# Performance work log

Measured on AMD Instinct MI355X. Metric: run time of the kernel, lower is better.

## Reference

```python
import jax, jax.numpy as jnp
import numpy as np
from jax import lax

EPS = 1e-5

def _dsconv(x, dw, pw, g, b, m, v, relu):
    # x: [B,C,H,W]; dw: [C,1,3,3] depthwise; pw: [C,C,1,1] pointwise; eval-mode BN
    C = x.shape[1]
    y = lax.conv_general_dilated(x, dw, (1, 1), 'SAME', feature_group_count=C)
    y = lax.conv_general_dilated(y, pw, (1, 1), 'SAME')
    scale = (g * lax.rsqrt(v + EPS))[None, :, None, None]
    y = y * scale + (b - m * g * lax.rsqrt(v + EPS))[None, :, None, None]
    return jnp.maximum(y, 0.0) if relu else y

def _attention(x, wq, bq, wk, bk, wv, bv, gamma):
    b, c, h, w = x.shape
    n = h * w
    xf = x.reshape(b, c, n)                      # [B,C,N]
    q = jnp.einsum('oc,bcn->bon', wq, xf) + bq[None, :, None]   # [B,C/8,N]
    k = jnp.einsum('oc,bcn->bon', wk, xf) + bk[None, :, None]   # [B,C/8,N]
    v = jnp.einsum('oc,bcn->bon', wv, xf) + bv[None, :, None]   # [B,C,N]
    logits = jnp.einsum('bdm,bdn->bmn', q, k)    # q^T k, [B,N,N]
    attn = jax.nn.softmax(logits, axis=2)
    out = jnp.einsum('bcn,bmn->bcm', v, attn).reshape(b, c, h, w)
    return gamma[0] * out + x

def setup_inputs() -> dict:
    key = jax.random.key(0)
    ks = jax.random.split(key, 20)
    B, C, H, W = 64, 256, 32, 32
    C8 = C // 8
    rn = lambda k, s, sc: (jax.random.normal(k, s, dtype=jnp.float32) * sc)
    return {
        'x': rn(ks[0], (B, C, H, W), 1.0),
        'dw1': rn(ks[1], (C, 1, 3, 3), 0.2),
        'pw1': rn(ks[2], (C, C, 1, 1), 0.06),
        'bn1_g': jax.random.uniform(ks[3], (C,), jnp.float32, 0.5, 1.5),
        'bn1_b': rn(ks[4], (C,), 0.1),
        'bn1_m': rn(ks[5], (C,), 0.1),
        'bn1_v': jax.random.uniform(ks[6], (C,), jnp.float32, 0.5, 1.5),
        'dw2': rn(ks[7], (C, 1, 3, 3), 0.2),
        'pw2': rn(ks[8], (C, C, 1, 1), 0.06),
        'bn2_g': jax.random.uniform(ks[9], (C,), jnp.float32, 0.5, 1.5),
        'bn2_b': rn(ks[10], (C,), 0.1),
        'bn2_m': rn(ks[11], (C,), 0.1),
        'bn2_v': jax.random.uniform(ks[12], (C,), jnp.float32, 0.5, 1.5),
        'wq': rn(ks[13], (C8, C), 0.06),
        'bq': rn(ks[14], (C8,), 0.02),
        'wk': rn(ks[15], (C8, C), 0.06),
        'bk': rn(ks[16], (C8,), 0.02),
        'wv': rn(ks[17], (C, C), 0.06),
        'bv': rn(ks[18], (C,), 0.02),
        'gamma': rn(ks[19], (1,), 0.5),
    }

def reference(x, dw1, pw1, bn1_g, bn1_b, bn1_m, bn1_v,
              dw2, pw2, bn2_g, bn2_b, bn2_m, bn2_v,
              wq, bq, wk, bk, wv, bv, gamma):
    out = _dsconv(x, dw1, pw1, bn1_g, bn1_b, bn1_m, bn1_v, relu=True)
    out = _dsconv(out, dw2, pw2, bn2_g, bn2_b, bn2_m, bn2_v, relu=False)
    out = _attention(out + x, wq, bq, wk, bk, wv, bv, gamma)
    return jnp.maximum(out, 0.0)
```

## Files before the change

### kernel.cpp

```cpp
#include <hip/hip_runtime.h>
#include <cstdint>
#include <cstddef>

#define B_ 64
#define C_ 256
#define N_ 1024
#define LOG2E 1.4426950408889634f

typedef short v8s __attribute__((ext_vector_type(8)));
typedef float v4f __attribute__((ext_vector_type(4)));
typedef unsigned int u32;
typedef unsigned short u16;

#define VMCNT(N) asm volatile("s_waitcnt vmcnt(" #N ")" ::: "memory")
#define LGKM0 asm volatile("s_waitcnt lgkmcnt(0)" ::: "memory")
#define SBAR __builtin_amdgcn_s_barrier()
#define SCHEDB __builtin_amdgcn_sched_barrier(0)

__device__ __forceinline__ float bf2f(u16 u) {
  return __uint_as_float(((u32)u) << 16);
}
__device__ __forceinline__ u16 f2bf(float f) {
  u32 x = __float_as_uint(f);
  x += 0x7fffu + ((x >> 16) & 1u);
  return (u16)(x >> 16);
}
__device__ __forceinline__ u32 pack2(float a, float b) {
  return (u32)f2bf(a) | ((u32)f2bf(b) << 16);
}
__device__ __forceinline__ u32 cvtpk(float lo, float hi) {
  u32 r;
  asm("v_cvt_pk_bf16_f32 %0, %1, %2" : "=v"(r) : "v"(lo), "v"(hi));
  return r;
}

typedef __attribute__((address_space(3))) unsigned int lds_as_t;
typedef __attribute__((address_space(1))) const unsigned int glb_as_t;
__device__ __forceinline__ void ld_lds16(const u16* g, u16* l) {
  __builtin_amdgcn_global_load_lds((glb_as_t*)g, (lds_as_t*)l, 16, 0, 0);
}

__global__ __launch_bounds__(256) void prep(
    const float* __restrict__ g1, const float* __restrict__ b1,
    const float* __restrict__ m1, const float* __restrict__ v1,
    const float* __restrict__ g2, const float* __restrict__ b2,
    const float* __restrict__ m2, const float* __restrict__ v2,
    const float* __restrict__ wq, const float* __restrict__ bq,
    const float* __restrict__ wk, const float* __restrict__ bk,
    const float* __restrict__ wv, const float* __restrict__ bv,
    const float* __restrict__ pw1, const float* __restrict__ pw2,
    const float* __restrict__ dw1, const float* __restrict__ dw2,
    float* __restrict__ scale1, float* __restrict__ shift1,
    float* __restrict__ scale2, float* __restrict__ shift2,
    float* __restrict__ dwT1, float* __restrict__ dwT2,
    u16* __restrict__ pw1b, u16* __restrict__ pw2b, u16* __restrict__ wcatb,
    float* __restrict__ bcat) {
  const int gt = blockIdx.x * 256 + threadIdx.x;
  if (gt < 256) {
    float s1 = g1[gt] * rsqrtf(v1[gt] + 1e-5f);
    scale1[gt] = s1;
    shift1[gt] = b1[gt] - m1[gt] * s1;
    float s2 = g2[gt] * rsqrtf(v2[gt] + 1e-5f);
    scale2[gt] = s2;
    shift2[gt] = b2[gt] - m2[gt] * s2;
  }
  if (gt < 320)
    bcat[gt] = (gt < 32) ? bq[gt] * LOG2E
                         : (gt < 64) ? bk[gt - 32] : bv[gt - 64];
  if (gt < 2304) {
    dwT1[(gt % 9) * 256 + gt / 9] = dw1[gt];
    dwT2[(gt % 9) * 256 + gt / 9] = dw2[gt];
  }
  for (int e = gt; e < 65536; e += 16384) {
    pw1b[e] = f2bf(pw1[e]);
    pw2b[e] = f2bf(pw2[e]);
  }
  for (int e = gt; e < 81920; e += 16384) {
    const int o = e >> 8;
    float w = (o < 32) ? wq[e] * LOG2E
                       : (o < 64) ? wk[e - 8192] : wv[e - 16384];
    wcatb[e] = f2bf(w);
  }
}

__global__ __launch_bounds__(256) void transpose_x(const float* __restrict__ x,
                                                   u16* __restrict__ xt) {
  __shared__ float t[64][65];
  const int b = blockIdx.z, c0 = blockIdx.y * 64, n0 = blockIdx.x * 64;
  const float* xp = x + ((size_t)b * C_ + c0) * N_ + n0;
  const int tn = threadIdx.x & 63, tc = threadIdx.x >> 6;
#pragma unroll
  for (int i = 0; i < 16; ++i)
    t[tc + 4 * i][tn] = xp[(size_t)(tc + 4 * i) * N_ + tn];
  __syncthreads();
  u16* op = xt + ((size_t)b * N_ + n0) * C_ + c0;
  const int oc = threadIdx.x & 63, on = threadIdx.x >> 6;
#pragma unroll
  for (int i = 0; i < 16; ++i)
    op[(size_t)(on + 4 * i) * C_ + oc] = f2bf(t[oc][on + 4 * i]);
}

__global__ __launch_bounds__(256) void dw_nhwc(const u16* __restrict__ src,
                                               const float* __restrict__ wT,
                                               u16* __restrict__ dst) {
  __shared__ float wl[9][256];
  const int b = blockIdx.y;
  for (int e = threadIdx.x; e < 2304; e += 256) wl[e >> 8][e & 255] = wT[e];
  __syncthreads();
  const int pl = threadIdx.x >> 5, c0 = (threadIdx.x & 31) * 8;
  const int p = blockIdx.x * 8 + pl;
  const int h = p >> 5, wx = p & 31;
  const u16* sp = src + (size_t)b * N_ * C_;
  float acc[8] = {0.f, 0.f, 0.f, 0.f, 0.f, 0.f, 0.f, 0.f};
#pragma unroll
  for (int dh = -1; dh <= 1; ++dh) {
    const int hh = h + dh;
    if (hh < 0 || hh > 31) continue;
#pragma unroll
    for (int dx = -1; dx <= 1; ++dx) {
      const int ww = wx + dx;
      if (ww < 0 || ww > 31) continue;
      const int k = (dh + 1) * 3 + (dx + 1);
      const uint4 v = *(const uint4*)(sp + (size_t)(hh * 32 + ww) * C_ + c0);
      const u32 vv[4] = {v.x, v.y, v.z, v.w};
#pragma unroll
      for (int j = 0; j < 4; ++j) {
        acc[2 * j] += bf2f((u16)(vv[j] & 0xffffu)) * wl[k][c0 + 2 * j];
        acc[2 * j + 1] += bf2f((u16)(vv[j] >> 16)) * wl[k][c0 + 2 * j + 1];
      }
    }
  }
  uint4 o4;
  o4.x = pack2(acc[0], acc[1]);
  o4.y = pack2(acc[2], acc[3]);
  o4.z = pack2(acc[4], acc[5]);
  o4.w = pack2(acc[6], acc[7]);
  *(uint4*)(dst + ((size_t)b * N_ + p) * C_ + c0) = o4;
}

template <int EPI>
__global__ __launch_bounds__(256, 4) void gemm(
    const u16* __restrict__ X, const u16* __restrict__ W,
    const float* __restrict__ scale, const float* __restrict__ shift,
    const u16* __restrict__ resid, u16* __restrict__ Y, u16* __restrict__ Y2) {
  __shared__ u16 smem[17408];
  u16(*Ys)[136] = (u16(*)[136])smem;
  u16(*YsQ)[68] = (u16(*)[68])smem;

  const int tid = threadIdx.x;
  const int b = blockIdx.z;
  const int n0 = blockIdx.x * 128, o0 = blockIdx.y * 128;
  const int wid = tid >> 6, lane = tid & 63;
  const int wn = wid & 1, wo = wid >> 1;
  const int l15 = lane & 15, l4 = lane >> 4;
  const int r16 = lane >> 2, c16 = (lane & 3) * 8;

  v4f acc[4][4];
#pragma unroll
  for (int i = 0; i < 4; ++i)
#pragma unroll
    for (int j = 0; j < 4; ++j) acc[i][j] = v4f{0.f, 0.f, 0.f, 0.f};

  auto stage = [&](int kidx, int bufsel) {
    const int k0 = (kidx & 7) * 32;
    u16* Xd = smem + bufsel * 8192;
    u16* Wd = Xd + 4096;
#pragma unroll
    for (int g = 0; g < 2; ++g) {
      const int base = wid * 32 + g * 16;
      ld_lds16(X + ((size_t)b * N_ + n0 + base + r16) * C_ + k0 + c16,
               Xd + base * 32);
      int wr = o0 + base + r16;
      if (EPI == 2 && wr > 319) wr = 319;
      ld_lds16(W + (size_t)wr * C_ + k0 + c16, Wd + base * 32);
    }
  };

  stage(0, 0);
  stage(1, 1);

#pragma unroll
  for (int k = 0; k < 8; ++k) {
    const int cur = k & 1;
    if (k < 7) {
      VMCNT(4);
    } else {
      VMCNT(0);
    }
    SCHEDB;
    SBAR;
    const u16(*Xs)[32] = (const u16(*)[32])(smem + cur * 8192);
    const u16(*Ws)[32] = (const u16(*)[32])(smem + cur * 8192 + 4096);
    v8s af[4], bf4[4];
#pragma unroll
    for (int f = 0; f < 4; ++f) {
      if constexpr (EPI != 2) {
        af[f] = *(const v8s*)&Ws[wo * 64 + f * 16 + l15][l4 * 8];
        bf4[f] = *(const v8s*)&Xs[wn * 64 + f * 16 + l15][l4 * 8];
      } else {
        af[f] = *(const v8s*)&Xs[wn * 64 + f * 16 + l15][l4 * 8];
        bf4[f] = *(const v8s*)&Ws[wo * 64 + f * 16 + l15][l4 * 8];
      }
    }
#pragma unroll
    for (int i = 0; i < 4; ++i)
#pragma unroll
      for (int j = 0; j < 4; ++j)
        acc[i][j] = __builtin_amdgcn_mfma_f32_16x16x32_bf16(af[i], bf4[j],
                                                            acc[i][j], 0, 0, 0);
    LGKM0;
    SBAR;
    SCHEDB;
    if (k < 6) stage(k + 2, cur);
  }

  if constexpr (EPI != 2) {
#pragma unroll
    for (int i = 0; i < 4; ++i) {
      const int oL = wo * 64 + i * 16 + l4 * 4;
      const int o = o0 + oL;
      const float4 sc = *(const float4*)&scale[o];
      const float4 sh = *(const float4*)&shift[o];
#pragma unroll
      for (int j = 0; j < 4; ++j) {
        const int nL = wn * 64 + j * 16 + l15;
        float y0 = acc[i][j][0] * sc.x + sh.x;
        float y1 = acc[i][j][1] * sc.y + sh.y;
        float y2 = acc[i][j][2] * sc.z + sh.z;
        float y3 = acc[i][j][3] * sc.w + sh.w;
        if constexpr (EPI == 0) {
          y0 = fmaxf(y0, 0.f);
          y1 = fmaxf(y1, 0.f);
          y2 = fmaxf(y2, 0.f);
          y3 = fmaxf(y3, 0.f);
        } else {
          const uint2 rb =
              *(const uint2*)(resid + ((size_t)b * N_ + n0 + nL) * C_ + o);
          y0 += bf2f((u16)(rb.x & 0xffffu));
          y1 += bf2f((u16)(rb.x >> 16));
          y2 += bf2f((u16)(rb.y & 0xffffu));
          y3 += bf2f((u16)(rb.y >> 16));
        }
        uint2 st;
        st.x = pack2(y0, y1);
        st.y = pack2(y2, y3);
        *(uint2*)&Ys[nL][oL] = st;
      }
    }
    __syncthreads();
#pragma unroll
    for (int s = 0; s < 8; ++s) {
      const int nL = s * 16 + (tid >> 4);
      const int slot = tid & 15;
      const uint4 v = *(const uint4*)&Ys[nL][slot * 8];
      *(uint4*)&Y[((size_t)b * N_ + n0 + nL) * C_ + o0 + slot * 8] = v;
    }
  } else {
    float bj[4];
#pragma unroll
    for (int j = 0; j < 4; ++j) {
      int o = o0 + wo * 64 + j * 16 + l15;
      bj[j] = shift[o > 319 ? 319 : o];
    }
    if (o0 == 0 && wo == 0) {
#pragma unroll
      for (int i = 0; i < 4; ++i) {
        const int nL = wn * 64 + i * 16 + l4 * 4;
#pragma unroll
        for (int j = 0; j < 4; ++j) {
          const int oL = j * 16 + l15;
#pragma unroll
          for (int r = 0; r < 4; ++r)
            YsQ[nL + r][oL] = f2bf(acc[i][j][r] + bj[j]);
        }
      }
    } else {
#pragma unroll
      for (int i = 0; i < 4; ++i) {
        const int nL = wn * 64 + i * 16 + l4 * 4;
#pragma unroll
        for (int j = 0; j < 4; ++j) {
          const int oL = wo * 64 + j * 16 + l15;
          uint2 st;
          st.x = pack2(acc[i][j][0] + bj[j], acc[i][j][1] + bj[j]);
          st.y = pack2(acc[i][j][2] + bj[j], acc[i][j][3] + bj[j]);
          *(uint2*)&Ys[oL][nL] = st;
        }
      }
    }
    __syncthreads();
    if (o0 == 0) {
#pragma unroll
      for (int s = 0; s < 4; ++s) {
        const int e = s * 256 + tid;
        const int row = e >> 3, seg = e & 7;
        const uint4 v = *(const uint4*)&YsQ[row][seg * 8];
        *(uint4*)&Y[((size_t)b * N_ + n0 + row) * 64 + seg * 8] = v;
      }
#pragma unroll
      for (int s = 0; s < 4; ++s) {
        const int e = s * 256 + tid;
        const int oL = 64 + (e >> 4), slot = e & 15;
        const uint4 v = *(const uint4*)&Ys[oL][slot * 8];
        *(uint4*)&Y2[((size_t)b * C_ + oL - 64) * N_ + n0 + slot * 8] = v;
      }
    } else {
#pragma unroll
      for (int s = 0; s < 8; ++s) {
        const int oL = s * 16 + (tid >> 4);
        const int c = o0 + oL - 64;
        if (c < 256) {
          const int slot = tid & 15;
          const uint4 v = *(const uint4*)&Ys[oL][slot * 8];
          *(uint4*)&Y2[((size_t)b * C_ + c) * N_ + n0 + slot * 8] = v;
        }
      }
    }
  }
}

__global__ __launch_bounds__(256, 3) void flash(
    const u16* __restrict__ qk, const u16* __restrict__ vchw,
    const u16* __restrict__ abf, const float* __restrict__ gamma_p,
    float* __restrict__ out) {
  const int b = blockIdx.x;
  const int m0 = blockIdx.y * 64;
  const int tid = threadIdx.x, wid = tid >> 6, lane = tid & 63;
  const int l15 = lane & 15, l4 = lane >> 4;
  const int mw = m0 + wid * 16;
  const int cq = wid * 64;

  __shared__ u16 Vs[256][64];
  __shared__ u16 Pl[2][64][72];
  __shared__ float Sl[64];

  const u16* qkb = qk + (size_t)b * N_ * 64;
  const u16* vb = vchw + (size_t)b * C_ * N_;
  const v8s qf = *(const v8s*)&qkb[(size_t)(mw + l15) * 64 + l4 * 8];

  const int s_row = lane >> 3;
  const int s_j = (lane & 7) ^ (s_row & 7);

#pragma unroll
  for (int g = 0; g < 8; ++g) {
    const int base = cq + g * 8;
    ld_lds16(vb + (size_t)(base + s_row) * N_ + s_j * 8, &Vs[base][0]);
  }

  float Mloc = -3e38f;
  {
    v8s kf[4];
#pragma unroll
    for (int f = 0; f < 4; ++f)
      kf[f] = *(const v8s*)&qkb[(size_t)(f * 16 + l15) * 64 + 32 + l4 * 8];
    for (int t = 0; t < 16; ++t) {
      v8s kn[4];
      if (t < 15) {
        const int n1 = (t + 1) * 64;
#pragma unroll
        for (int f = 0; f < 4; ++f)
          kn[f] =
              *(const v8s*)&qkb[(size_t)(n1 + f * 16 + l15) * 64 + 32 + l4 * 8];
      }
#pragma unroll
      for (int f = 0; f < 4; ++f) {
        const v4f lt = __builtin_amdgcn_mfma_f32_16x16x32_bf16(
            kf[f], qf, v4f{0.f, 0.f, 0.f, 0.f}, 0, 0, 0);
        Mloc = fmaxf(Mloc, fmaxf(fmaxf(lt[0], lt[1]), fmaxf(lt[2], lt[3])));
      }
      if (t < 15) {
#pragma unroll
        for (int f = 0; f < 4; ++f) kf[f] = kn[f];
      }
    }
  }
  Mloc = fmaxf(Mloc, __shfl_xor(Mloc, 16));
  Mloc = fmaxf(Mloc, __shfl_xor(Mloc, 32));
  const float M = Mloc;

  v4f acc[4][4];
#pragma unroll
  for (int mf = 0; mf < 4; ++mf)
#pragma unroll
    for (int j = 0; j < 4; ++j) acc[mf][j] = v4f{0.f, 0.f, 0.f, 0.f};
  float S0 = 0.f, S1 = 0.f, S2 = 0.f, S3 = 0.f;
  v8s kf[4];
#pragma unroll
  for (int f = 0; f < 4; ++f)
    kf[f] = *(const v8s*)&qkb[(size_t)(f * 16 + l15) * 64 + 32 + l4 * 8];
  VMCNT(0);

  for (int t = 0; t < 16; ++t) {
    const int tb = t & 1;
    v4f lt[4];
#pragma unroll
    for (int f = 0; f < 4; ++f)
      lt[f] = __builtin_amdgcn_mfma_f32_16x16x32_bf16(
          kf[f], qf, v4f{0.f, 0.f, 0.f, 0.f}, 0, 0, 0);
#pragma unroll
    for (int f = 0; f < 4; ++f) {
      const float p0 = exp2f(lt[f][0] - M);
      const float p1 = exp2f(lt[f][1] - M);
      const float p2 = exp2f(lt[f][2] - M);
      const float p3 = exp2f(lt[f][3] - M);
      S0 += p0;
      S1 += p1;
      S2 += p2;
      S3 += p3;
      uint2 pw;
      pw.x = cvtpk(p0, p1);
      pw.y = cvtpk(p2, p3);
      *(uint2*)&Pl[tb][wid * 16 + l15][f * 16 + l4 * 4] = pw;
    }
    SCHEDB;
    {
      const int n1 = ((t + 1) & 15) * 64;
#pragma unroll
      for (int f = 0; f < 4; ++f)
        kf[f] =
            *(const v8s*)&qkb[(size_t)(n1 + f * 16 + l15) * 64 + 32 + l4 * 8];
    }
    SCHEDB;
    LGKM0;
    SBAR;
    VMCNT(4);
    SCHEDB;
    __builtin_amdgcn_s_setprio(1);
#pragma unroll
    for (int ks = 0; ks < 2; ++ks) {
      v8s pa[4];
#pragma unroll
      for (int mf = 0; mf < 4; ++mf)
        pa[mf] = *(const v8s*)&Pl[tb][mf * 16 + l15][ks * 32 + l4 * 8];
#pragma unroll
      for (int j = 0; j < 4; ++j) {
        const int col = 8 * (((ks * 4) + l4) ^ (l15 & 7));
        const v8s vf = *(const v8s*)&Vs[cq + j * 16 + l15][col];
#pragma unroll
        for (int mf = 0; mf < 4; ++mf)
          acc[mf][j] = __builtin_amdgcn_mfma_f32_16x16x32_bf16(
              pa[mf], vf, acc[mf][j], 0, 0, 0);
      }
    }
    __builtin_amdgcn_s_setprio(0);
    SCHEDB;
    {
      const int n1 = ((t + 1) & 15) * 64;
#pragma unroll
      for (int g = 0; g < 8; ++g) {
        const int base = cq + g * 8;
        ld_lds16(vb + (size_t)(base + s_row) * N_ + n1 + s_j * 8, &Vs[base][0]);
      }
    }
    SCHEDB;
  }

  float S = (S0 + S1) + (S2 + S3);
  S += __shfl_xor(S, 16);
  S += __shfl_xor(S, 32);
  if (lane < 16) Sl[wid * 16 + lane] = 1.f / S;
  __syncthreads();

  const float gma = gamma_p[0];
  float invv[4][4];
#pragma unroll
  for (int mf = 0; mf < 4; ++mf)
#pragma unroll
    for (int r = 0; r < 4; ++r) invv[mf][r] = Sl[mf * 16 + l4 * 4 + r];

#pragma unroll
  for (int mf = 0; mf < 4; ++mf) {
    const int mb = m0 + mf * 16 + l4 * 4;
#pragma unroll
    for (int j = 0; j < 4; ++j) {
      const int c = cq + j * 16 + l15;
      float4 y;
      float* yp = (float*)&y;
#pragma unroll
      for (int r = 0; r < 4; ++r) {
        const float av = bf2f(abf[((size_t)b * N_ + mb + r) * C_ + c]);
        yp[r] = fmaxf(gma * acc[mf][j][r] * invv[mf][r] + av, 0.f);
      }
      *(float4*)&out[((size_t)b * C_ + c) * N_ + mb] = y;
    }
  }
}

extern "C" void kernel_launch(void* const* d_in, const int* in_sizes, int n_in,
                              void* d_out, int out_size, void* d_ws,
                              size_t ws_size, hipStream_t stream) {
  const float* x = (const float*)d_in[0];
  const float* dw1 = (const float*)d_in[1];
  const float* pw1 = (const float*)d_in[2];
  const float* bn1g = (const float*)d_in[3];
  const float* bn1b = (const float*)d_in[4];
  const float* bn1m = (const float*)d_in[5];
  const float* bn1v = (const float*)d_in[6];
  const float* dw2 = (const float*)d_in[7];
  const float* pw2 = (const float*)d_in[8];
  const float* bn2g = (const float*)d_in[9];
  const float* bn2b = (const float*)d_in[10];
  const float* bn2m = (const float*)d_in[11];
  const float* bn2v = (const float*)d_in[12];
  const float* wq = (const float*)d_in[13];
  const float* bq = (const float*)d_in[14];
  const float* wk = (const float*)d_in[15];
  const float* bk = (const float*)d_in[16];
  const float* wv = (const float*)d_in[17];
  const float* bv = (const float*)d_in[18];
  const float* gamma = (const float*)d_in[19];
  float* out = (float*)d_out;

  char* ws = (char*)d_ws;
  size_t off = 0;
  auto alloc = [&](size_t bytes) {
    void* p = ws + off;
    off += (bytes + 255) & ~(size_t)255;
    return p;
  };
  const size_t NE = (size_t)B_ * N_ * C_;

  u16* bufA = (u16*)alloc(NE * 2);
  u16* bufB = (u16*)alloc(NE * 2);
  u16* bufC = (u16*)alloc(NE * 2);
  u16* abf = (u16*)alloc(NE * 2);
  float* scale1 = (float*)alloc(256 * 4);
  float* shift1 = (float*)alloc(256 * 4);
  float* scale2 = (float*)alloc(256 * 4);
  float* shift2 = (float*)alloc(256 * 4);
  float* dwT1 = (float*)alloc(2304 * 4);
  float* dwT2 = (float*)alloc(2304 * 4);
  u16* pw1b = (u16*)alloc(65536 * 2);
  u16* pw2b = (u16*)alloc(65536 * 2);
  u16* wcatb = (u16*)alloc(81920 * 2);
  float* bcat = (float*)alloc(384 * 4);

  u16* xt = bufA;
  u16* t1 = bufB;
  u16* y1 = bufC;
  u16* t2 = bufB;
  u16* qkbuf = bufC;
  u16* vchw = bufA;

  prep<<<64, 256, 0, stream>>>(bn1g, bn1b, bn1m, bn1v, bn2g, bn2b, bn2m, bn2v,
                               wq, bq, wk, bk, wv, bv, pw1, pw2, dw1, dw2,
                               scale1, shift1, scale2, shift2, dwT1, dwT2,
                               pw1b, pw2b, wcatb, bcat);
  transpose_x<<<dim3(16, 4, B_), 256, 0, stream>>>(x, xt);
  dw_nhwc<<<dim3(128, B_), 256, 0, stream>>>(xt, dwT1, t1);
  gemm<0><<<dim3(8, 2, B_), 256, 0, stream>>>(t1, pw1b, scale1, shift1,
                                              nullptr, y1, nullptr);
  dw_nhwc<<<dim3(128, B_), 256, 0, stream>>>(y1, dwT2, t2);
  gemm<1><<<dim3(8, 2, B_), 256, 0, stream>>>(t2, pw2b, scale2, shift2, xt,
                                              abf, nullptr);
  gemm<2><<<dim3(8, 3, B_), 256, 0, stream>>>(abf, wcatb, nullptr, bcat,
                                              nullptr, qkbuf, vchw);
  flash<<<dim3(64, 16), 256, 0, stream>>>(qkbuf, vchw, abf, gamma, out);
}
```

Measured before the change: 256.3 us.

## Software-pipeline attention PV loop: overlap next-tile softmax with current PV MFMAs

Restructures the attention main loop into a prologue/steady-state/epilogue pipeline. Each iteration computes the logits for tile t, then issues the PV MFMAs for tile t-1 from the other P buffer, then does exp and writes P for tile t. The first V tile load is deferred until after the first logits so it overlaps the max pass. The aim is to hide exp/VALU latency and barrier stalls behind matrix work. In exchange the waitcnt accounting gets more delicate and register pressure from the live logits rises.

```diff
diff --git a/kernel.cpp b/kernel.cpp
--- a/kernel.cpp
+++ b/kernel.cpp
@@ -341,18 +341,12 @@
   const int s_row = lane >> 3;
   const int s_j = (lane & 7) ^ (s_row & 7);
 
-#pragma unroll
-  for (int g = 0; g < 8; ++g) {
-    const int base = cq + g * 8;
-    ld_lds16(vb + (size_t)(base + s_row) * N_ + s_j * 8, &Vs[base][0]);
-  }
-
   float Mloc = -3e38f;
   {
-    v8s kf[4];
+    v8s kf1[4];
 #pragma unroll
     for (int f = 0; f < 4; ++f)
-      kf[f] = *(const v8s*)&qkb[(size_t)(f * 16 + l15) * 64 + 32 + l4 * 8];
+      kf1[f] = *(const v8s*)&qkb[(size_t)(f * 16 + l15) * 64 + 32 + l4 * 8];
     for (int t = 0; t < 16; ++t) {
       v8s kn[4];
       if (t < 15) {
@@ -365,12 +359,12 @@
 #pragma unroll
       for (int f = 0; f < 4; ++f) {
         const v4f lt = __builtin_amdgcn_mfma_f32_16x16x32_bf16(
-            kf[f], qf, v4f{0.f, 0.f, 0.f, 0.f}, 0, 0, 0);
+            kf1[f], qf, v4f{0.f, 0.f, 0.f, 0.f}, 0, 0, 0);
         Mloc = fmaxf(Mloc, fmaxf(fmaxf(lt[0], lt[1]), fmaxf(lt[2], lt[3])));
       }
       if (t < 15) {
 #pragma unroll
-        for (int f = 0; f < 4; ++f) kf[f] = kn[f];
+        for (int f = 0; f < 4; ++f) kf1[f] = kn[f];
       }
     }
   }
@@ -389,9 +383,9 @@
   for (int f = 0; f < 4; ++f)
     kf[f] = *(const v8s*)&qkb[(size_t)(f * 16 + l15) * 64 + 32 + l4 * 8];
   VMCNT(0);
-
-  for (int t = 0; t < 16; ++t) {
-    const int tb = t & 1;
+  SCHEDB;
+
+  {
     v4f lt[4];
 #pragma unroll
     for (int f = 0; f < 4; ++f)
@@ -410,9 +404,65 @@
       uint2 pw;
       pw.x = cvtpk(p0, p1);
       pw.y = cvtpk(p2, p3);
-      *(uint2*)&Pl[tb][wid * 16 + l15][f * 16 + l4 * 4] = pw;
-    }
+      *(uint2*)&Pl[0][wid * 16 + l15][f * 16 + l4 * 4] = pw;
+    }
+#pragma unroll
+    for (int f = 0; f < 4; ++f)
+      kf[f] = *(const v8s*)&qkb[(size_t)(64 + f * 16 + l15) * 64 + 32 + l4 * 8];
     SCHEDB;
+#pragma unroll
+    for (int g = 0; g < 8; ++g) {
+      const int base = cq + g * 8;
+      ld_lds16(vb + (size_t)(base + s_row) * N_ + s_j * 8, &Vs[base][0]);
+    }
+    LGKM0;
+    SBAR;
+  }
+
+  for (int t = 1; t < 16; ++t) {
+    const int pb = (t - 1) & 1, cb = t & 1;
+    VMCNT(8);
+    SCHEDB;
+    v4f lt[4];
+#pragma unroll
+    for (int f = 0; f < 4; ++f)
+      lt[f] = __builtin_amdgcn_mfma_f32_16x16x32_bf16(
+          kf[f], qf, v4f{0.f, 0.f, 0.f, 0.f}, 0, 0, 0);
+    VMCNT(0);
+    SCHEDB;
+    __builtin_amdgcn_s_setprio(1);
+#pragma unroll
+    for (int ks = 0; ks < 2; ++ks) {
+      v8s pa[4];
+#pragma unroll
+      for (int mf = 0; mf < 4; ++mf)
+        pa[mf] = *(const v8s*)&Pl[pb][mf * 16 + l15][ks * 32 + l4 * 8];
+#pragma unroll
+      for (int j = 0; j < 4; ++j) {
+        const int col = 8 * (((ks * 4) + l4) ^ (l15 & 7));
+        const v8s vf = *(const v8s*)&Vs[cq + j * 16 + l15][col];
+#pragma unroll
+        for (int mf = 0; mf < 4; ++mf)
+          acc[mf][j] = __builtin_amdgcn_mfma_f32_16x16x32_bf16(
+              pa[mf], vf, acc[mf][j], 0, 0, 0);
+      }
+    }
+    __builtin_amdgcn_s_setprio(0);
+#pragma unroll
+    for (int f = 0; f < 4; ++f) {
+      const float p0 = exp2f(lt[f][0] - M);
+      const float p1 = exp2f(lt[f][1] - M);
+      const float p2 = exp2f(lt[f][2] - M);
+      const float p3 = exp2f(lt[f][3] - M);
+      S0 += p0;
+      S1 += p1;
+      S2 += p2;
+      S3 += p3;
+      uint2 pw;
+      pw.x = cvtpk(p0, p1);
+      pw.y = cvtpk(p2, p3);
+      *(uint2*)&Pl[cb][wid * 16 + l15][f * 16 + l4 * 4] = pw;
+    }
     {
       const int n1 = ((t + 1) & 15) * 64;
 #pragma unroll
@@ -421,39 +471,38 @@
             *(const v8s*)&qkb[(size_t)(n1 + f * 16 + l15) * 64 + 32 + l4 * 8];
     }
     SCHEDB;
-    LGKM0;
-    SBAR;
-    VMCNT(4);
-    SCHEDB;
-    __builtin_amdgcn_s_setprio(1);
-#pragma unroll
-    for (int ks = 0; ks < 2; ++ks) {
-      v8s pa[4];
-#pragma unroll
-      for (int mf = 0; mf < 4; ++mf)
-        pa[mf] = *(const v8s*)&Pl[tb][mf * 16 + l15][ks * 32 + l4 * 8];
-#pragma unroll
-      for (int j = 0; j < 4; ++j) {
-        const int col = 8 * (((ks * 4) + l4) ^ (l15 & 7));
-        const v8s vf = *(const v8s*)&Vs[cq + j * 16 + l15][col];
-#pragma unroll
-        for (int mf = 0; mf < 4; ++mf)
-          acc[mf][j] = __builtin_amdgcn_mfma_f32_16x16x32_bf16(
-              pa[mf], vf, acc[mf][j], 0, 0, 0);
-      }
-    }
-    __builtin_amdgcn_s_setprio(0);
-    SCHEDB;
     {
-      const int n1 = ((t + 1) & 15) * 64;
+      const int n1 = t * 64;
 #pragma unroll
       for (int g = 0; g < 8; ++g) {
         const int base = cq + g * 8;
         ld_lds16(vb + (size_t)(base + s_row) * N_ + n1 + s_j * 8, &Vs[base][0]);
       }
     }
-    SCHEDB;
-  }
+    LGKM0;
+    SBAR;
+  }
+
+  VMCNT(0);
+  SCHEDB;
+  __builtin_amdgcn_s_setprio(1);
+#pragma unroll
+  for (int ks = 0; ks < 2; ++ks) {
+    v8s pa[4];
+#pragma unroll
+    for (int mf = 0; mf < 4; ++mf)
+      pa[mf] = *(const v8s*)&Pl[1][mf * 16 + l15][ks * 32 + l4 * 8];
+#pragma unroll
+    for (int j = 0; j < 4; ++j) {
+      const int col = 8 * (((ks * 4) + l4) ^ (l15 & 7));
+      const v8s vf = *(const v8s*)&Vs[cq + j * 16 + l15][col];
+#pragma unroll
+      for (int mf = 0; mf < 4; ++mf)
+        acc[mf][j] = __builtin_amdgcn_mfma_f32_16x16x32_bf16(
+            pa[mf], vf, acc[mf][j], 0, 0, 0);
+    }
+  }
+  __builtin_amdgcn_s_setprio(0);
 
   float S = (S0 + S1) + (S2 + S3);
   S += __shfl_xor(S, 16);
```

After: 252.0 us. No clear change (-1.7%).
